# Performance work log

Measured on AMD Instinct MI355X. Metric: run time of the kernel, lower is better.

## Reference

```python
import jax, jax.numpy as jnp
import numpy as np
import math

H = 1024
N = 64
DT_MIN, DT_MAX = 1e-3, 1e-1
L_SEQ = 4096


def setup_inputs() -> dict:
    key = jax.random.key(0)
    k1, k2, k3 = jax.random.split(key, 3)
    # C ~ complex normal, stored as (..., 2) real view like torch.view_as_real
    C = jax.random.normal(k1, (H, N // 2, 2), dtype=jnp.float32)
    # log_dt ~ U[log(dt_min), log(dt_max)]
    log_dt = jax.random.uniform(k2, (H,), dtype=jnp.float32) * (
        math.log(DT_MAX) - math.log(DT_MIN)
    ) + math.log(DT_MIN)
    # log_A_real = log(0.5), A_imag = pi * arange(N/2) repeated over H
    log_A_real = jnp.full((H, N // 2), math.log(0.5), dtype=jnp.float32)
    A_imag = math.pi * jnp.broadcast_to(
        jnp.arange(N // 2, dtype=jnp.float32), (H, N // 2)
    )
    return {"C": C, "log_dt": log_dt, "log_A_real": log_A_real, "A_imag": A_imag, "L": L_SEQ}


def reference(C, log_dt, log_A_real, A_imag, L):
    dt = jnp.exp(log_dt)                                  # (H,)
    Cc = jax.lax.complex(C[..., 0], C[..., 1])            # (H, N/2) complex
    A = -jnp.exp(log_A_real) + 1j * A_imag                # (H, N/2) complex
    dtA = A * dt[:, None]                                 # (H, N/2)
    # Vandermonde: exp(dtA * l) for l in [0, L)
    K = dtA[:, :, None] * jnp.arange(L, dtype=jnp.float32)  # (H, N/2, L)
    Cm = Cc * (jnp.exp(dtA) - 1.0) / A                    # (H, N/2)
    K = 2.0 * jnp.einsum("hn,hnl->hl", Cm, jnp.exp(K)).real  # (H, L)
    return K
```

## Files before the change

### kernel.cpp

```cpp
#include <hip/hip_runtime.h>
#include <hip/hip_bf16.h>
#include <math.h>


#define H_DIM 1024
#define NH 32
#define L_DIM 4096
#define SPLIT 2
#define L_BLK (L_DIM / SPLIT)
#define TPB 256
#define PER 8
#define NTA 32
#define NTB 8
#define STRIDE_F 84

__global__ __launch_bounds__(TPB, 8) void s4d_kernel(
    const float* __restrict__ C,
    const float* __restrict__ log_dt,
    const float* __restrict__ log_A_real,
    const float* __restrict__ A_imag,
    float* __restrict__ out)
{
    const int h   = blockIdx.x;
    const int off = blockIdx.y * L_BLK;
    const int t   = threadIdx.x;

    __shared__ float lds[NH * STRIDE_F];

    const double INV_2PI = 0.15915494309189533576888376337251;

    {
        const int n = t & 31;
        const int s = t >> 5;

        const float dtf = __expf(log_dt[h]);
        const float arf = -__expf(log_A_real[h * NH + n]);
        const float aif = A_imag[h * NH + n];
        const float are = arf * dtf;
        const double th_rev = (double)aif * (double)dtf * INV_2PI;

        const float mw = __expf(are);
        const float u1 = (float)(th_rev - floor(th_rev));
        const float wr = mw * __builtin_amdgcn_cosf(u1);
        const float wi = mw * __builtin_amdgcn_sinf(u1);

        const float cr = C[(h * NH + n) * 2 + 0];
        const float ci = C[(h * NH + n) * 2 + 1];
        const float er = wr - 1.0f;
        const float ei = wi;
        const float tr = cr * er - ci * ei;
        const float ti = cr * ei + ci * er;
        const float inv = 2.0f / (arf * arf + aif * aif);
        const float cmr = (tr * arf + ti * aif) * inv;
        const float cmi = (ti * arf - tr * aif) * inv;

        float* base = &lds[n * STRIDE_F];

#pragma unroll
        for (int k = 0; k < 4; ++k) {
            const int i = s + 8 * k;
            const int l = off + 8 * i;
            const float mag = __expf(are * (float)l);
            double u = (double)l * th_rev;
            u -= floor(u);
            const float uf = (float)u;
            const float br = mag * __builtin_amdgcn_cosf(uf);
            const float bi = mag * __builtin_amdgcn_sinf(uf);
            base[4 + 2 * i]     = cmr * br - cmi * bi;
            base[4 + 2 * i + 1] = cmr * bi + cmi * br;
        }
        {
            const int l = 256 * s;
            const float mag = __expf(are * (float)l);
            double u = (double)l * th_rev;
            u -= floor(u);
            const float uf = (float)u;
            base[68 + 2 * s]     = mag * __builtin_amdgcn_cosf(uf);
            base[68 + 2 * s + 1] = mag * __builtin_amdgcn_sinf(uf);
        }
        if (s == 0) {
            base[0] = wr;
            base[1] = wi;
            base[2] = wr + wr;
            base[3] = -__expf(are + are);
        }
    }
    __syncthreads();

    float acc[PER];
#pragma unroll
    for (int j = 0; j < PER; ++j) acc[j] = 0.0f;

    const int ia = t & 31;
    const int ib = t >> 5;

#pragma unroll 4
    for (int n = 0; n < NH; ++n) {
        const float* base = &lds[n * STRIDE_F];
        const float4 hdr = *(const float4*)base;
        const float2 ta  = *(const float2*)(base + 4 + 2 * ia);
        const float2 tb  = *(const float2*)(base + 68 + 2 * ib);

        const float zr = ta.x * tb.x - ta.y * tb.y;
        const float zi = ta.x * tb.y + ta.y * tb.x;

        float x0 = zr;
        float x1 = zr * hdr.x - zi * hdr.y;
        acc[0] += x0;
        acc[1] += x1;
        float tq = hdr.w * x0;
#pragma unroll
        for (int j = 2; j < PER; ++j) {
            const float x2 = fmaf(hdr.z, x1, tq);
            tq = hdr.w * x1;
            acc[j] += x2;
            x0 = x1;
            x1 = x2;
        }
    }

    float4* op = (float4*)(out + (size_t)h * L_DIM + off + t * PER);
#pragma unroll
    for (int j = 0; j < PER / 4; ++j) {
        op[j] = make_float4(acc[4 * j], acc[4 * j + 1], acc[4 * j + 2], acc[4 * j + 3]);
    }
}

extern "C" void kernel_launch(void* const* d_in, const int* in_sizes, int n_in,
                              void* d_out, int out_size, void* d_ws, size_t ws_size,
                              hipStream_t stream) {
    const float* C          = (const float*)d_in[0];
    const float* log_dt     = (const float*)d_in[1];
    const float* log_A_real = (const float*)d_in[2];
    const float* A_imag     = (const float*)d_in[3];
    float* out = (float*)d_out;

    s4d_kernel<<<dim3(H_DIM, SPLIT), dim3(TPB), 0, stream>>>(C, log_dt, log_A_real, A_imag, out);
}
```

Before: 79.06 us.

## Process full sequence per block with two interleaved 8-chains using packed float2 math

Drops the L split so each block covers all 4096 outputs for one head. Each thread now computes 16 consecutive outputs as two 8-element Chebyshev-style recurrences, seeded 8 apart through an extra w^8 twiddle. The two chains run in lockstep in 2-wide vector registers so the compiler can emit packed FMA. This halves the per-block twiddle setup relative to total work and cuts the grid in half, at the cost of more registers per thread (launch bounds drop from 8 to 4) and fewer blocks.

```diff
diff --git a/kernel.cpp b/kernel.cpp
--- a/kernel.cpp
+++ b/kernel.cpp
@@ -6,24 +6,27 @@
 #define H_DIM 1024
 #define NH 32
 #define L_DIM 4096
-#define SPLIT 2
-#define L_BLK (L_DIM / SPLIT)
 #define TPB 256
-#define PER 8
-#define NTA 32
-#define NTB 8
-#define STRIDE_F 84
+#define CHUNK 8
+#define STRIDE_F 72
 
-__global__ __launch_bounds__(TPB, 8) void s4d_kernel(
+typedef float v2f __attribute__((ext_vector_type(2)));
+
+#if defined(__has_builtin) && __has_builtin(__builtin_elementwise_fma)
+#define V2FMA(a, b, c) __builtin_elementwise_fma((a), (b), (c))
+#else
+#define V2FMA(a, b, c) ((a) * (b) + (c))
+#endif
+
+__global__ __launch_bounds__(TPB, 4) void s4d_kernel(
     const float* __restrict__ C,
     const float* __restrict__ log_dt,
     const float* __restrict__ log_A_real,
     const float* __restrict__ A_imag,
     float* __restrict__ out)
 {
-    const int h   = blockIdx.x;
-    const int off = blockIdx.y * L_BLK;
-    const int t   = threadIdx.x;
+    const int h = blockIdx.x;
+    const int t = threadIdx.x;
 
     __shared__ float lds[NH * STRIDE_F];
 
@@ -57,73 +60,85 @@
         float* base = &lds[n * STRIDE_F];
 
 #pragma unroll
-        for (int k = 0; k < 4; ++k) {
+        for (int k = 0; k < 2; ++k) {
             const int i = s + 8 * k;
-            const int l = off + 8 * i;
+            const int l = 16 * i;
             const float mag = __expf(are * (float)l);
             double u = (double)l * th_rev;
             u -= floor(u);
             const float uf = (float)u;
             const float br = mag * __builtin_amdgcn_cosf(uf);
             const float bi = mag * __builtin_amdgcn_sinf(uf);
-            base[4 + 2 * i]     = cmr * br - cmi * bi;
-            base[4 + 2 * i + 1] = cmr * bi + cmi * br;
+            base[6 + 2 * i]     = cmr * br - cmi * bi;
+            base[6 + 2 * i + 1] = cmr * bi + cmi * br;
         }
-        {
-            const int l = 256 * s;
+#pragma unroll
+        for (int k = 0; k < 2; ++k) {
+            const int i = s + 8 * k;
+            const int l = 256 * i;
             const float mag = __expf(are * (float)l);
             double u = (double)l * th_rev;
             u -= floor(u);
             const float uf = (float)u;
-            base[68 + 2 * s]     = mag * __builtin_amdgcn_cosf(uf);
-            base[68 + 2 * s + 1] = mag * __builtin_amdgcn_sinf(uf);
+            base[38 + 2 * i]     = mag * __builtin_amdgcn_cosf(uf);
+            base[38 + 2 * i + 1] = mag * __builtin_amdgcn_sinf(uf);
         }
         if (s == 0) {
             base[0] = wr;
             base[1] = wi;
             base[2] = wr + wr;
             base[3] = -__expf(are + are);
+            const float m8 = __expf(are * 8.0f);
+            double u8 = th_rev * 8.0;
+            u8 -= floor(u8);
+            const float uf8 = (float)u8;
+            base[4] = m8 * __builtin_amdgcn_cosf(uf8);
+            base[5] = m8 * __builtin_amdgcn_sinf(uf8);
         }
     }
     __syncthreads();
 
-    float acc[PER];
+    v2f acc[CHUNK];
 #pragma unroll
-    for (int j = 0; j < PER; ++j) acc[j] = 0.0f;
+    for (int j = 0; j < CHUNK; ++j) acc[j] = (v2f){0.0f, 0.0f};
 
-    const int ia = t & 31;
-    const int ib = t >> 5;
+    const int ia = t & 15;
+    const int ib = t >> 4;
 
 #pragma unroll 4
     for (int n = 0; n < NH; ++n) {
         const float* base = &lds[n * STRIDE_F];
-        const float4 hdr = *(const float4*)base;
-        const float2 ta  = *(const float2*)(base + 4 + 2 * ia);
-        const float2 tb  = *(const float2*)(base + 68 + 2 * ib);
+        const float4 h4 = *(const float4*)base;
+        const float2 w8 = *(const float2*)(base + 4);
+        const float2 ta = *(const float2*)(base + 6 + 2 * ia);
+        const float2 tb = *(const float2*)(base + 38 + 2 * ib);
 
-        const float zr = ta.x * tb.x - ta.y * tb.y;
-        const float zi = ta.x * tb.y + ta.y * tb.x;
+        const float zr  = ta.x * tb.x - ta.y * tb.y;
+        const float zi  = ta.x * tb.y + ta.y * tb.x;
+        const float zbr = zr * w8.x - zi * w8.y;
+        const float zbi = zr * w8.y + zi * w8.x;
 
-        float x0 = zr;
-        float x1 = zr * hdr.x - zi * hdr.y;
+        v2f x0 = {zr, zbr};
+        v2f x1 = {zr * h4.x - zi * h4.y, zbr * h4.x - zbi * h4.y};
         acc[0] += x0;
         acc[1] += x1;
-        float tq = hdr.w * x0;
+        const v2f p2 = {h4.z, h4.z};
+        const v2f q2 = {h4.w, h4.w};
+        v2f tq = q2 * x0;
 #pragma unroll
-        for (int j = 2; j < PER; ++j) {
-            const float x2 = fmaf(hdr.z, x1, tq);
-            tq = hdr.w * x1;
+        for (int j = 2; j < CHUNK; ++j) {
+            const v2f x2 = V2FMA(p2, x1, tq);
+            tq = q2 * x1;
             acc[j] += x2;
-            x0 = x1;
             x1 = x2;
         }
     }
 
-    float4* op = (float4*)(out + (size_t)h * L_DIM + off + t * PER);
-#pragma unroll
-    for (int j = 0; j < PER / 4; ++j) {
-        op[j] = make_float4(acc[4 * j], acc[4 * j + 1], acc[4 * j + 2], acc[4 * j + 3]);
-    }
+    float4* op = (float4*)(out + (size_t)h * L_DIM + t * 16);
+    op[0] = make_float4(acc[0].x, acc[1].x, acc[2].x, acc[3].x);
+    op[1] = make_float4(acc[4].x, acc[5].x, acc[6].x, acc[7].x);
+    op[2] = make_float4(acc[0].y, acc[1].y, acc[2].y, acc[3].y);
+    op[3] = make_float4(acc[4].y, acc[5].y, acc[6].y, acc[7].y);
 }
 
 extern "C" void kernel_launch(void* const* d_in, const int* in_sizes, int n_in,
@@ -135,5 +150,5 @@
     const float* A_imag     = (const float*)d_in[3];
     float* out = (float*)d_out;
 
-    s4d_kernel<<<dim3(H_DIM, SPLIT), dim3(TPB), 0, stream>>>(C, log_dt, log_A_real, A_imag, out);
+    s4d_kernel<<<dim3(H_DIM), dim3(TPB), 0, stream>>>(C, log_dt, log_A_real, A_imag, out);
 }
```

New measurement: 76.86 us (median of 2 runs). -2.8%, faster.
